# Kernel optimization log

Measured on AMD Instinct MI355X. Metric: run time of the kernel, lower is better.

## Reference

```python
import jax, jax.numpy as jnp
import numpy as np

N, E, F, H = 50000, 1_600_000, 6, 64


def setup_inputs() -> dict:
    key = jax.random.key(0)
    ks = jax.random.split(key, 12)
    inp = {
        "vertex_features": jax.random.normal(ks[0], (N, F), dtype=jnp.float32),
        "edges": jax.random.randint(ks[1], (2, E), 0, N, dtype=jnp.int64 if jax.config.jax_enable_x64 else jnp.int32),
        "weights": jax.random.uniform(ks[2], (E,), dtype=jnp.float32),
        # GCNConv layer params (glorot-ish scale) + biases (PyG default bias=True)
        "W1": jax.random.normal(ks[3], (F, H), dtype=jnp.float32) / np.sqrt(F),
        "b1": jnp.zeros((H,), jnp.float32),
        "W2": jax.random.normal(ks[4], (H, H), dtype=jnp.float32) / np.sqrt(H),
        "b2": jnp.zeros((H,), jnp.float32),
        "W3": jax.random.normal(ks[5], (H, H), dtype=jnp.float32) / np.sqrt(H),
        "b3": jnp.zeros((H,), jnp.float32),
        "Wl": jax.random.normal(ks[6], (H, 1), dtype=jnp.float32) / np.sqrt(H),
        "bl": jnp.zeros((1,), jnp.float32),
    }
    return inp


def _gcn_norm(edges, weights, n):
    # PyG gcn_norm: add self loops (weight 1), symmetric D^-1/2 A D^-1/2;
    # degree computed at target nodes (edge_index[1], flow source_to_target).
    row, col = edges[0], edges[1]
    loop = jnp.arange(n, dtype=row.dtype)
    row_f = jnp.concatenate([row, loop])
    col_f = jnp.concatenate([col, loop])
    w_f = jnp.concatenate([weights, jnp.ones((n,), weights.dtype)])
    deg = jax.ops.segment_sum(w_f, col_f, num_segments=n)
    dis = jnp.where(deg > 0, jax.lax.rsqrt(jnp.maximum(deg, 1e-30)), 0.0)
    norm = dis[row_f] * w_f * dis[col_f]
    return row_f, col_f, norm


def _gcn_conv(x, W, b, row, col, norm, n):
    xw = x @ W                                   # [n, H_out]
    agg = jax.ops.segment_sum(norm[:, None] * xw[row], col, num_segments=n)
    return agg + b


def reference(vertex_features, edges, weights, W1, b1, W2, b2, W3, b3, Wl, bl):
    n = vertex_features.shape[0]
    row, col, norm = _gcn_norm(edges, weights, n)  # norm identical for all layers
    h = jax.nn.sigmoid(_gcn_conv(vertex_features, W1, b1, row, col, norm, n))
    h = jax.nn.sigmoid(_gcn_conv(h, W2, b2, row, col, norm, n))
    h = jax.nn.sigmoid(_gcn_conv(h, W3, b3, row, col, norm, n))
    logits = h @ Wl + bl                           # [n, 1]
    return jax.nn.softmax(logits, axis=0)          # softmax over node dim
```

## Files before the change

kernel.cpp:

```cpp
#include <hip/hip_runtime.h>
#include <math.h>


#define BLK 256
#define SKB 256
#define CHUNK 4096
#define LROW 72

typedef __attribute__((ext_vector_type(8))) short bf16x8;
typedef __attribute__((ext_vector_type(4))) float f32x4;

__device__ inline unsigned short f2bf(float f) {
  unsigned u = __float_as_uint(f);
  return (unsigned short)((u + 0x7FFF + ((u >> 16) & 1)) >> 16);
}
__device__ inline float bflo(unsigned u) { return __uint_as_float(u << 16); }
__device__ inline float bfhi(unsigned u) { return __uint_as_float(u & 0xFFFF0000u); }


__global__ __launch_bounds__(256) void k_binscatter(
    const int* __restrict__ row, const int* __restrict__ col,
    const float* __restrict__ w, int E,
    int* __restrict__ bfill, int2* __restrict__ bucket, int CAP, int nEB,
    const float* __restrict__ W2, const float* __restrict__ W3,
    unsigned short* __restrict__ W2b, unsigned short* __restrict__ W3b) {
  if (blockIdx.x >= nEB) {
    int i = (blockIdx.x - nEB) * BLK + threadIdx.x;
    if (i < 4096) { W2b[i] = f2bf(W2[i]); W3b[i] = f2bf(W3[i]); }
    return;
  }
  __shared__ int2 stage[CHUNK];
  __shared__ int lhist[SKB], lbase[SKB], gbase[SKB], lfill[SKB];
  int t = threadIdx.x;
  int e0 = blockIdx.x * CHUNK;
  int n = E - e0; if (n > CHUNK) n = CHUNK;
  lhist[t] = 0; lfill[t] = 0;
  __syncthreads();
  for (int i = t; i < n; i += BLK) atomicAdd(&lhist[((unsigned)col[e0 + i]) >> 8], 1);
  __syncthreads();
  lbase[t] = lhist[t];
  __syncthreads();
  for (int off = 1; off < SKB; off <<= 1) {
    int v = (t >= off) ? lbase[t - off] : 0;
    __syncthreads();
    lbase[t] += v;
    __syncthreads();
  }
  int excl = lbase[t] - lhist[t];
  int cb = lhist[t];
  gbase[t] = cb ? atomicAdd(&bfill[t << 4], cb) : 0;
  __syncthreads();
  lbase[t] = excl;
  __syncthreads();
  for (int i = t; i < n; i += BLK) {
    int c = col[e0 + i];
    int b = ((unsigned)c) >> 8;
    int r = atomicAdd(&lfill[b], 1);
    stage[lbase[b] + r] = make_int2(row[e0 + i] | (c << 16), __float_as_int(w[e0 + i]));
  }
  __syncthreads();
  for (int i = t; i < n; i += BLK) {
    int2 p = stage[i];
    int b = ((unsigned)p.x) >> 24;
    bucket[(size_t)b * CAP + gbase[b] + (i - lbase[b])] = p;
  }
}


__global__ __launch_bounds__(256) void k_build(
    const int2* __restrict__ bucket, const int* __restrict__ bfill,
    const float* __restrict__ x,
    unsigned* __restrict__ csr, int* __restrict__ cnt, int* __restrict__ start,
    float* __restrict__ dis, unsigned short* __restrict__ x8b, int CAP, int N) {
  __shared__ int   hist[SKB];
  __shared__ float wsum[SKB];
  __shared__ int   lstart[SKB + 1];
  __shared__ int   lfill[SKB];
  int b = blockIdx.x, t = threadIdx.x;
  int n0 = b << 8;
  int M = N - n0; if (M > 256) M = 256;
  if (M <= 0) return;
  hist[t] = 0; wsum[t] = 0.0f; lfill[t] = 0;
  __syncthreads();
  const int2* bb = bucket + (size_t)b * CAP;
  int ec = bfill[b << 4];
  for (int i = t; i < ec; i += BLK) {
    int2 p = bb[i];
    int lc = (((unsigned)p.x) >> 16) & 255;
    atomicAdd(&hist[lc], 1);
    atomicAdd(&wsum[lc], __int_as_float(p.y));
  }
  __syncthreads();
  if (t == 0) {
    int run = 0;
    for (int i = 0; i < M; ++i) { lstart[i] = run; run += hist[i]; }
    lstart[M] = run;
  }
  __syncthreads();
  if (t < M) {
    int n = n0 + t;
    cnt[n] = hist[t];
    start[n] = b * CAP + lstart[t];
    float d = 1.0f / sqrtf(wsum[t] + 1.0f);
    dis[n] = d;
    const float* xr = x + (size_t)n * 6;
    uint4 pk;
    pk.x = (unsigned)f2bf(d * xr[0]) | ((unsigned)f2bf(d * xr[1]) << 16);
    pk.y = (unsigned)f2bf(d * xr[2]) | ((unsigned)f2bf(d * xr[3]) << 16);
    pk.z = (unsigned)f2bf(d * xr[4]) | ((unsigned)f2bf(d * xr[5]) << 16);
    pk.w = 0u;
    *(uint4*)(x8b + (size_t)n * 8) = pk;
  }
  __syncthreads();
  for (int i = t; i < ec; i += BLK) {
    int2 p = bb[i];
    int lc = (((unsigned)p.x) >> 16) & 255;
    int pos = lstart[lc] + atomicAdd(&lfill[lc], 1);
    csr[(size_t)b * CAP + pos] =
        ((unsigned)p.x & 0xFFFFu) | ((unsigned)f2bf(__int_as_float(p.y)) << 16);
  }
}


__global__ void k_layer1(const unsigned short* __restrict__ x8b,
                         const int* __restrict__ start, const int* __restrict__ cnt,
                         const unsigned* __restrict__ csr, const float* __restrict__ dis,
                         const float* __restrict__ W1, const float* __restrict__ b1,
                         unsigned short* __restrict__ hb, int N) {
  int t = blockIdx.x * blockDim.x + threadIdx.x;
  int n = t >> 3, sub = t & 7;
  if (n >= N) return;
  float a0 = 0.f, a1 = 0.f, a2 = 0.f, a3 = 0.f, a4 = 0.f, a5 = 0.f;
  if (sub == 0) {
    uint4 sv = *(const uint4*)(x8b + (size_t)n * 8);
    a0 = bflo(sv.x); a1 = bfhi(sv.x); a2 = bflo(sv.y);
    a3 = bfhi(sv.y); a4 = bflo(sv.z); a5 = bfhi(sv.z);
  }
  int s = start[n], e = s + cnt[n];
  int i = s + sub;
  for (; i + 8 < e; i += 16) {
    unsigned p0 = csr[i], p1 = csr[i + 8];
    uint4 h0 = *(const uint4*)(x8b + (size_t)(p0 & 0xFFFFu) * 8);
    uint4 h1 = *(const uint4*)(x8b + (size_t)(p1 & 0xFFFFu) * 8);
    float v0 = bfhi(p0), v1 = bfhi(p1);
    a0 += v0 * bflo(h0.x) + v1 * bflo(h1.x);
    a1 += v0 * bfhi(h0.x) + v1 * bfhi(h1.x);
    a2 += v0 * bflo(h0.y) + v1 * bflo(h1.y);
    a3 += v0 * bfhi(h0.y) + v1 * bfhi(h1.y);
    a4 += v0 * bflo(h0.z) + v1 * bflo(h1.z);
    a5 += v0 * bfhi(h0.z) + v1 * bfhi(h1.z);
  }
  for (; i < e; i += 8) {
    unsigned pe = csr[i];
    float v = bfhi(pe);
    uint4 hv = *(const uint4*)(x8b + (size_t)(pe & 0xFFFFu) * 8);
    a0 += v * bflo(hv.x); a1 += v * bfhi(hv.x);
    a2 += v * bflo(hv.y); a3 += v * bfhi(hv.y);
    a4 += v * bflo(hv.z); a5 += v * bfhi(hv.z);
  }
#pragma unroll
  for (int m = 1; m < 8; m <<= 1) {
    a0 += __shfl_xor(a0, m, 64); a1 += __shfl_xor(a1, m, 64);
    a2 += __shfl_xor(a2, m, 64); a3 += __shfl_xor(a3, m, 64);
    a4 += __shfl_xor(a4, m, 64); a5 += __shfl_xor(a5, m, 64);
  }
  float d = dis[n];
  a0 *= d; a1 *= d; a2 *= d; a3 *= d; a4 *= d; a5 *= d;
  unsigned short* o = hb + (size_t)n * 64;
#pragma unroll
  for (int jj = 0; jj < 2; ++jj) {
    int j4 = sub * 2 + jj;
    float4 acc = *(const float4*)(b1 + j4 * 4);
    const float* Wc = W1 + j4 * 4;
    acc.x += a0*Wc[0] + a1*Wc[64] + a2*Wc[128] + a3*Wc[192] + a4*Wc[256] + a5*Wc[320];
    acc.y += a0*Wc[1] + a1*Wc[65] + a2*Wc[129] + a3*Wc[193] + a4*Wc[257] + a5*Wc[321];
    acc.z += a0*Wc[2] + a1*Wc[66] + a2*Wc[130] + a3*Wc[194] + a4*Wc[258] + a5*Wc[322];
    acc.w += a0*Wc[3] + a1*Wc[67] + a2*Wc[131] + a3*Wc[195] + a4*Wc[259] + a5*Wc[323];
    uint2 pk;
    pk.x = (unsigned)f2bf(d / (1.0f + expf(-acc.x))) |
           ((unsigned)f2bf(d / (1.0f + expf(-acc.y))) << 16);
    pk.y = (unsigned)f2bf(d / (1.0f + expf(-acc.z))) |
           ((unsigned)f2bf(d / (1.0f + expf(-acc.w))) << 16);
    *(uint2*)(o + j4 * 4) = pk;
  }
}


__device__ inline void agg16(const unsigned short* __restrict__ hb,
                             const int* __restrict__ start,
                             const int* __restrict__ cnt,
                             const unsigned* __restrict__ csr,
                             const float* __restrict__ dis,
                             unsigned short* lag, int n0, int N) {
  int t = threadIdx.x;
  int r = t >> 4, sub = t & 15;
  int n = n0 + r;
  uint2 pk = make_uint2(0u, 0u);
  if (n < N) {
    uint2 sv = *(const uint2*)(hb + (size_t)n * 64 + sub * 4);
    float a0 = bflo(sv.x), a1 = bfhi(sv.x), a2 = bflo(sv.y), a3 = bfhi(sv.y);
    int s = start[n], e = s + cnt[n];
    int i = s;
    for (; i + 8 <= e; i += 8) {
      unsigned p0 = csr[i],     p1 = csr[i + 1], p2 = csr[i + 2], p3 = csr[i + 3];
      unsigned p4 = csr[i + 4], p5 = csr[i + 5], p6 = csr[i + 6], p7 = csr[i + 7];
      uint2 h0 = *(const uint2*)(hb + (size_t)(p0 & 0xFFFFu) * 64 + sub * 4);
      uint2 h1 = *(const uint2*)(hb + (size_t)(p1 & 0xFFFFu) * 64 + sub * 4);
      uint2 h2 = *(const uint2*)(hb + (size_t)(p2 & 0xFFFFu) * 64 + sub * 4);
      uint2 h3 = *(const uint2*)(hb + (size_t)(p3 & 0xFFFFu) * 64 + sub * 4);
      uint2 h4 = *(const uint2*)(hb + (size_t)(p4 & 0xFFFFu) * 64 + sub * 4);
      uint2 h5 = *(const uint2*)(hb + (size_t)(p5 & 0xFFFFu) * 64 + sub * 4);
      uint2 h6 = *(const uint2*)(hb + (size_t)(p6 & 0xFFFFu) * 64 + sub * 4);
      uint2 h7 = *(const uint2*)(hb + (size_t)(p7 & 0xFFFFu) * 64 + sub * 4);
      float v0 = bfhi(p0), v1 = bfhi(p1), v2 = bfhi(p2), v3 = bfhi(p3);
      float v4 = bfhi(p4), v5 = bfhi(p5), v6 = bfhi(p6), v7 = bfhi(p7);
      a0 += v0*bflo(h0.x) + v1*bflo(h1.x) + v2*bflo(h2.x) + v3*bflo(h3.x)
          + v4*bflo(h4.x) + v5*bflo(h5.x) + v6*bflo(h6.x) + v7*bflo(h7.x);
      a1 += v0*bfhi(h0.x) + v1*bfhi(h1.x) + v2*bfhi(h2.x) + v3*bfhi(h3.x)
          + v4*bfhi(h4.x) + v5*bfhi(h5.x) + v6*bfhi(h6.x) + v7*bfhi(h7.x);
      a2 += v0*bflo(h0.y) + v1*bflo(h1.y) + v2*bflo(h2.y) + v3*bflo(h3.y)
          + v4*bflo(h4.y) + v5*bflo(h5.y) + v6*bflo(h6.y) + v7*bflo(h7.y);
      a3 += v0*bfhi(h0.y) + v1*bfhi(h1.y) + v2*bfhi(h2.y) + v3*bfhi(h3.y)
          + v4*bfhi(h4.y) + v5*bfhi(h5.y) + v6*bfhi(h6.y) + v7*bfhi(h7.y);
    }
    for (; i < e; ++i) {
      unsigned pe = csr[i];
      float v = bfhi(pe);
      uint2 hv = *(const uint2*)(hb + (size_t)(pe & 0xFFFFu) * 64 + sub * 4);
      a0 += v * bflo(hv.x); a1 += v * bfhi(hv.x);
      a2 += v * bflo(hv.y); a3 += v * bfhi(hv.y);
    }
    float d = dis[n];
    pk.x = (unsigned)f2bf(d * a0) | ((unsigned)f2bf(d * a1) << 16);
    pk.y = (unsigned)f2bf(d * a2) | ((unsigned)f2bf(d * a3) << 16);
  }
  *(uint2*)(lag + r * LROW + sub * 4) = pk;
}


__global__ __launch_bounds__(256) void k_layer2f(
    const unsigned short* __restrict__ hb_in,
    const int* __restrict__ start, const int* __restrict__ cnt,
    const unsigned* __restrict__ csr, const float* __restrict__ dis,
    const unsigned short* __restrict__ Wb, const float* __restrict__ b,
    unsigned short* __restrict__ hb_out, int N) {
  __shared__ unsigned short lag[16 * LROW];
  int n0 = blockIdx.x * 16;
  agg16(hb_in, start, cnt, csr, dis, lag, n0, N);
  __syncthreads();
  int t = threadIdx.x;
  int wid = t >> 6, lane = t & 63, quad = lane >> 4, r16 = lane & 15;
  bf16x8 Af0 = *(const bf16x8*)(lag + r16 * LROW + quad * 8);
  bf16x8 Af1 = *(const bf16x8*)(lag + r16 * LROW + 32 + quad * 8);
  bf16x8 Bf0, Bf1;
#pragma unroll
  for (int j = 0; j < 8; ++j) {
    Bf0[j] = (short)Wb[(quad * 8 + j) * 64 + wid * 16 + r16];
    Bf1[j] = (short)Wb[(32 + quad * 8 + j) * 64 + wid * 16 + r16];
  }
  f32x4 z = {0.f, 0.f, 0.f, 0.f};
  z = __builtin_amdgcn_mfma_f32_16x16x32_bf16(Af0, Bf0, z, 0, 0, 0);
  z = __builtin_amdgcn_mfma_f32_16x16x32_bf16(Af1, Bf1, z, 0, 0, 0);
  float bias = b[wid * 16 + r16];
#pragma unroll
  for (int reg = 0; reg < 4; ++reg) {
    int nb = n0 + quad * 4 + reg;
    if (nb < N) {
      float h = dis[nb] / (1.0f + expf(-(z[reg] + bias)));
      hb_out[(size_t)nb * 64 + wid * 16 + r16] = f2bf(h);
    }
  }
}


__global__ __launch_bounds__(256) void k_layer3f(
    const unsigned short* __restrict__ hb_in,
    const int* __restrict__ start, const int* __restrict__ cnt,
    const unsigned* __restrict__ csr, const float* __restrict__ dis,
    const unsigned short* __restrict__ Wb, const float* __restrict__ b,
    const float* __restrict__ Wl, const float* __restrict__ bl,
    float* __restrict__ expv, float* __restrict__ red_part, int N) {
  __shared__ unsigned short lag[16 * LROW];
  __shared__ float psum[16][4];
  int n0 = blockIdx.x * 16;
  agg16(hb_in, start, cnt, csr, dis, lag, n0, N);
  __syncthreads();
  int t = threadIdx.x;
  int wid = t >> 6, lane = t & 63, quad = lane >> 4, r16 = lane & 15;
  bf16x8 Af0 = *(const bf16x8*)(lag + r16 * LROW + quad * 8);
  bf16x8 Af1 = *(const bf16x8*)(lag + r16 * LROW + 32 + quad * 8);
  bf16x8 Bf0, Bf1;
#pragma unroll
  for (int j = 0; j < 8; ++j) {
    Bf0[j] = (short)Wb[(quad * 8 + j) * 64 + wid * 16 + r16];
    Bf1[j] = (short)Wb[(32 + quad * 8 + j) * 64 + wid * 16 + r16];
  }
  f32x4 z = {0.f, 0.f, 0.f, 0.f};
  z = __builtin_amdgcn_mfma_f32_16x16x32_bf16(Af0, Bf0, z, 0, 0, 0);
  z = __builtin_amdgcn_mfma_f32_16x16x32_bf16(Af1, Bf1, z, 0, 0, 0);
  float bias = b[wid * 16 + r16];
  float wl = Wl[wid * 16 + r16];
  float p[4];
#pragma unroll
  for (int reg = 0; reg < 4; ++reg)
    p[reg] = wl / (1.0f + expf(-(z[reg] + bias)));
#pragma unroll
  for (int m = 1; m < 16; m <<= 1) {
#pragma unroll
    for (int reg = 0; reg < 4; ++reg) p[reg] += __shfl_xor(p[reg], m, 64);
  }
  if (r16 == 0) {
#pragma unroll
    for (int reg = 0; reg < 4; ++reg) psum[quad * 4 + reg][wid] = p[reg];
  }
  __syncthreads();
  if (t < 16) {
    int n = n0 + t;
    float lg = psum[t][0] + psum[t][1] + psum[t][2] + psum[t][3] + bl[0];
    float ev = (n < N) ? expf(lg) : 0.f;
    if (n < N) expv[n] = ev;
#pragma unroll
    for (int m = 1; m < 16; m <<= 1) ev += __shfl_xor(ev, m, 64);
    if (t == 0) atomicAdd(&red_part[(blockIdx.x & 63) << 4], ev);
  }
}

__global__ void k_out(const float* __restrict__ expv, int N,
                      const float* __restrict__ red_part, float* __restrict__ out) {
  int i = blockIdx.x * blockDim.x + threadIdx.x;
  int lane = threadIdx.x & 63;
  float s = red_part[lane << 4];
#pragma unroll
  for (int o = 32; o > 0; o >>= 1) s += __shfl_down(s, o, 64);
  s = __shfl(s, 0, 64);
  if (i < N) out[i] = expv[i] / s;
}


extern "C" void kernel_launch(void* const* d_in, const int* in_sizes, int n_in,
                              void* d_out, int out_size, void* d_ws, size_t ws_size,
                              hipStream_t stream) {
  const float* x   = (const float*)d_in[0];
  const int*   edg = (const int*)d_in[1];
  const float* w   = (const float*)d_in[2];
  const float* W1  = (const float*)d_in[3];
  const float* b1  = (const float*)d_in[4];
  const float* W2  = (const float*)d_in[5];
  const float* b2  = (const float*)d_in[6];
  const float* W3  = (const float*)d_in[7];
  const float* b3  = (const float*)d_in[8];
  const float* Wl  = (const float*)d_in[9];
  const float* bl  = (const float*)d_in[10];
  float* out = (float*)d_out;

  const int N = in_sizes[0] / 6;
  const int E = in_sizes[2];
  const int* row = edg;
  const int* col = edg + E;
  const int NB = (N + 255) >> 8;

  size_t off = 0;
  char* base = (char*)d_ws;
  auto alloc = [&](size_t bytes) -> void* {
    void* p = base + off;
    off += (bytes + 255) & ~(size_t)255;
    return p;
  };
  int*   bfill    = (int*)alloc((size_t)SKB * 16 * 4);
  float* red_part = (float*)alloc((size_t)64 * 16 * 4);
  size_t zero_bytes = off;
  int*   cnt    = (int*)alloc((size_t)N * 4);
  int*   start  = (int*)alloc((size_t)N * 4);
  float* dis    = (float*)alloc((size_t)N * 4);
  float* expv   = (float*)alloc((size_t)N * 4);
  unsigned short* x8b = (unsigned short*)alloc((size_t)N * 8 * 2);
  unsigned short* hb  = (unsigned short*)alloc((size_t)N * 64 * 2);
  unsigned short* W2b = (unsigned short*)alloc(4096 * 2);
  unsigned short* W3b = (unsigned short*)alloc(4096 * 2);
  size_t remain = (ws_size > off) ? (ws_size - off) : 0;
  long long capn = ((long long)remain) / ((long long)NB * 12);
  int CAP = (int)capn;
  if (CAP > 9216) CAP = 9216;
  if (CAP < 8704) CAP = 8704;
  unsigned* csr = (unsigned*)alloc((size_t)NB * CAP * 4);
  size_t h2sz = (size_t)N * 64 * 2;
  size_t bksz = (size_t)NB * CAP * 8;
  void* shared_blk = alloc(h2sz > bksz ? h2sz : bksz);
  int2*           bucket = (int2*)shared_blk;
  unsigned short* hb2    = (unsigned short*)shared_blk;

  const int nEB = (E + CHUNK - 1) / CHUNK;
  const int gE  = nEB + 16;
  const int gN  = (N + BLK - 1) / BLK;
  const int gN8 = (N * 8 + BLK - 1) / BLK;
  const int g16 = (N + 15) / 16;

  hipMemsetAsync(d_ws, 0, zero_bytes, stream);

  k_binscatter<<<gE, BLK, 0, stream>>>(row, col, w, E, bfill, bucket, CAP,
                                       nEB, W2, W3, W2b, W3b);
  k_build     <<<NB, BLK, 0, stream>>>(bucket, bfill, x, csr, cnt, start, dis, x8b, CAP, N);

  k_layer1<<<gN8, BLK, 0, stream>>>(x8b, start, cnt, csr, dis, W1, b1, hb, N);

  k_layer2f<<<g16, BLK, 0, stream>>>(hb, start, cnt, csr, dis, W2b, b2, hb2, N);

  k_layer3f<<<g16, BLK, 0, stream>>>(hb2, start, cnt, csr, dis, W3b, b3,
                                     Wl, bl, expv, red_part, N);

  k_out<<<gN, BLK, 0, stream>>>(expv, N, red_part, out);
}
```

Measured before the change: 216.3 us.

## Fuse all GCN stages into one persistent kernel with grid-wide barriers

Replaces the six separate kernel launches (bin scatter, CSR build, three layers, softmax output) with a single persistent kernel that loops over work with grid-stride loops and synchronises phases through an atomic-counter grid barrier. The grid is sized from the occupancy API so that all blocks can be resident at once. CHUNK is halved so the shared-memory union fits the requested occupancy. This removes launch gaps and inter-kernel drain, but adds spin-barrier cost, relies on every block being co-resident to avoid deadlock, and may reduce per-phase parallelism compared with the original grids.

```diff
diff --git a/kernel.cpp b/kernel.cpp
--- a/kernel.cpp
+++ b/kernel.cpp
@@ -4,7 +4,7 @@
 
 #define BLK 256
 #define SKB 256
-#define CHUNK 4096
+#define CHUNK 2048
 #define LROW 72
 
 typedef __attribute__((ext_vector_type(8))) short bf16x8;
@@ -16,174 +16,6 @@
 }
 __device__ inline float bflo(unsigned u) { return __uint_as_float(u << 16); }
 __device__ inline float bfhi(unsigned u) { return __uint_as_float(u & 0xFFFF0000u); }
-
-
-__global__ __launch_bounds__(256) void k_binscatter(
-    const int* __restrict__ row, const int* __restrict__ col,
-    const float* __restrict__ w, int E,
-    int* __restrict__ bfill, int2* __restrict__ bucket, int CAP, int nEB,
-    const float* __restrict__ W2, const float* __restrict__ W3,
-    unsigned short* __restrict__ W2b, unsigned short* __restrict__ W3b) {
-  if (blockIdx.x >= nEB) {
-    int i = (blockIdx.x - nEB) * BLK + threadIdx.x;
-    if (i < 4096) { W2b[i] = f2bf(W2[i]); W3b[i] = f2bf(W3[i]); }
-    return;
-  }
-  __shared__ int2 stage[CHUNK];
-  __shared__ int lhist[SKB], lbase[SKB], gbase[SKB], lfill[SKB];
-  int t = threadIdx.x;
-  int e0 = blockIdx.x * CHUNK;
-  int n = E - e0; if (n > CHUNK) n = CHUNK;
-  lhist[t] = 0; lfill[t] = 0;
-  __syncthreads();
-  for (int i = t; i < n; i += BLK) atomicAdd(&lhist[((unsigned)col[e0 + i]) >> 8], 1);
-  __syncthreads();
-  lbase[t] = lhist[t];
-  __syncthreads();
-  for (int off = 1; off < SKB; off <<= 1) {
-    int v = (t >= off) ? lbase[t - off] : 0;
-    __syncthreads();
-    lbase[t] += v;
-    __syncthreads();
-  }
-  int excl = lbase[t] - lhist[t];
-  int cb = lhist[t];
-  gbase[t] = cb ? atomicAdd(&bfill[t << 4], cb) : 0;
-  __syncthreads();
-  lbase[t] = excl;
-  __syncthreads();
-  for (int i = t; i < n; i += BLK) {
-    int c = col[e0 + i];
-    int b = ((unsigned)c) >> 8;
-    int r = atomicAdd(&lfill[b], 1);
-    stage[lbase[b] + r] = make_int2(row[e0 + i] | (c << 16), __float_as_int(w[e0 + i]));
-  }
-  __syncthreads();
-  for (int i = t; i < n; i += BLK) {
-    int2 p = stage[i];
-    int b = ((unsigned)p.x) >> 24;
-    bucket[(size_t)b * CAP + gbase[b] + (i - lbase[b])] = p;
-  }
-}
-
-
-__global__ __launch_bounds__(256) void k_build(
-    const int2* __restrict__ bucket, const int* __restrict__ bfill,
-    const float* __restrict__ x,
-    unsigned* __restrict__ csr, int* __restrict__ cnt, int* __restrict__ start,
-    float* __restrict__ dis, unsigned short* __restrict__ x8b, int CAP, int N) {
-  __shared__ int   hist[SKB];
-  __shared__ float wsum[SKB];
-  __shared__ int   lstart[SKB + 1];
-  __shared__ int   lfill[SKB];
-  int b = blockIdx.x, t = threadIdx.x;
-  int n0 = b << 8;
-  int M = N - n0; if (M > 256) M = 256;
-  if (M <= 0) return;
-  hist[t] = 0; wsum[t] = 0.0f; lfill[t] = 0;
-  __syncthreads();
-  const int2* bb = bucket + (size_t)b * CAP;
-  int ec = bfill[b << 4];
-  for (int i = t; i < ec; i += BLK) {
-    int2 p = bb[i];
-    int lc = (((unsigned)p.x) >> 16) & 255;
-    atomicAdd(&hist[lc], 1);
-    atomicAdd(&wsum[lc], __int_as_float(p.y));
-  }
-  __syncthreads();
-  if (t == 0) {
-    int run = 0;
-    for (int i = 0; i < M; ++i) { lstart[i] = run; run += hist[i]; }
-    lstart[M] = run;
-  }
-  __syncthreads();
-  if (t < M) {
-    int n = n0 + t;
-    cnt[n] = hist[t];
-    start[n] = b * CAP + lstart[t];
-    float d = 1.0f / sqrtf(wsum[t] + 1.0f);
-    dis[n] = d;
-    const float* xr = x + (size_t)n * 6;
-    uint4 pk;
-    pk.x = (unsigned)f2bf(d * xr[0]) | ((unsigned)f2bf(d * xr[1]) << 16);
-    pk.y = (unsigned)f2bf(d * xr[2]) | ((unsigned)f2bf(d * xr[3]) << 16);
-    pk.z = (unsigned)f2bf(d * xr[4]) | ((unsigned)f2bf(d * xr[5]) << 16);
-    pk.w = 0u;
-    *(uint4*)(x8b + (size_t)n * 8) = pk;
-  }
-  __syncthreads();
-  for (int i = t; i < ec; i += BLK) {
-    int2 p = bb[i];
-    int lc = (((unsigned)p.x) >> 16) & 255;
-    int pos = lstart[lc] + atomicAdd(&lfill[lc], 1);
-    csr[(size_t)b * CAP + pos] =
-        ((unsigned)p.x & 0xFFFFu) | ((unsigned)f2bf(__int_as_float(p.y)) << 16);
-  }
-}
-
-
-__global__ void k_layer1(const unsigned short* __restrict__ x8b,
-                         const int* __restrict__ start, const int* __restrict__ cnt,
-                         const unsigned* __restrict__ csr, const float* __restrict__ dis,
-                         const float* __restrict__ W1, const float* __restrict__ b1,
-                         unsigned short* __restrict__ hb, int N) {
-  int t = blockIdx.x * blockDim.x + threadIdx.x;
-  int n = t >> 3, sub = t & 7;
-  if (n >= N) return;
-  float a0 = 0.f, a1 = 0.f, a2 = 0.f, a3 = 0.f, a4 = 0.f, a5 = 0.f;
-  if (sub == 0) {
-    uint4 sv = *(const uint4*)(x8b + (size_t)n * 8);
-    a0 = bflo(sv.x); a1 = bfhi(sv.x); a2 = bflo(sv.y);
-    a3 = bfhi(sv.y); a4 = bflo(sv.z); a5 = bfhi(sv.z);
-  }
-  int s = start[n], e = s + cnt[n];
-  int i = s + sub;
-  for (; i + 8 < e; i += 16) {
-    unsigned p0 = csr[i], p1 = csr[i + 8];
-    uint4 h0 = *(const uint4*)(x8b + (size_t)(p0 & 0xFFFFu) * 8);
-    uint4 h1 = *(const uint4*)(x8b + (size_t)(p1 & 0xFFFFu) * 8);
-    float v0 = bfhi(p0), v1 = bfhi(p1);
-    a0 += v0 * bflo(h0.x) + v1 * bflo(h1.x);
-    a1 += v0 * bfhi(h0.x) + v1 * bfhi(h1.x);
-    a2 += v0 * bflo(h0.y) + v1 * bflo(h1.y);
-    a3 += v0 * bfhi(h0.y) + v1 * bfhi(h1.y);
-    a4 += v0 * bflo(h0.z) + v1 * bflo(h1.z);
-    a5 += v0 * bfhi(h0.z) + v1 * bfhi(h1.z);
-  }
-  for (; i < e; i += 8) {
-    unsigned pe = csr[i];
-    float v = bfhi(pe);
-    uint4 hv = *(const uint4*)(x8b + (size_t)(pe & 0xFFFFu) * 8);
-    a0 += v * bflo(hv.x); a1 += v * bfhi(hv.x);
-    a2 += v * bflo(hv.y); a3 += v * bfhi(hv.y);
-    a4 += v * bflo(hv.z); a5 += v * bfhi(hv.z);
-  }
-#pragma unroll
-  for (int m = 1; m < 8; m <<= 1) {
-    a0 += __shfl_xor(a0, m, 64); a1 += __shfl_xor(a1, m, 64);
-    a2 += __shfl_xor(a2, m, 64); a3 += __shfl_xor(a3, m, 64);
-    a4 += __shfl_xor(a4, m, 64); a5 += __shfl_xor(a5, m, 64);
-  }
-  float d = dis[n];
-  a0 *= d; a1 *= d; a2 *= d; a3 *= d; a4 *= d; a5 *= d;
-  unsigned short* o = hb + (size_t)n * 64;
-#pragma unroll
-  for (int jj = 0; jj < 2; ++jj) {
-    int j4 = sub * 2 + jj;
-    float4 acc = *(const float4*)(b1 + j4 * 4);
-    const float* Wc = W1 + j4 * 4;
-    acc.x += a0*Wc[0] + a1*Wc[64] + a2*Wc[128] + a3*Wc[192] + a4*Wc[256] + a5*Wc[320];
-    acc.y += a0*Wc[1] + a1*Wc[65] + a2*Wc[129] + a3*Wc[193] + a4*Wc[257] + a5*Wc[321];
-    acc.z += a0*Wc[2] + a1*Wc[66] + a2*Wc[130] + a3*Wc[194] + a4*Wc[258] + a5*Wc[322];
-    acc.w += a0*Wc[3] + a1*Wc[67] + a2*Wc[131] + a3*Wc[195] + a4*Wc[259] + a5*Wc[323];
-    uint2 pk;
-    pk.x = (unsigned)f2bf(d / (1.0f + expf(-acc.x))) |
-           ((unsigned)f2bf(d / (1.0f + expf(-acc.y))) << 16);
-    pk.y = (unsigned)f2bf(d / (1.0f + expf(-acc.z))) |
-           ((unsigned)f2bf(d / (1.0f + expf(-acc.w))) << 16);
-    *(uint2*)(o + j4 * 4) = pk;
-  }
-}
 
 
 __device__ inline void agg16(const unsigned short* __restrict__ hb,
@@ -238,102 +70,277 @@
 }
 
 
-__global__ __launch_bounds__(256) void k_layer2f(
-    const unsigned short* __restrict__ hb_in,
-    const int* __restrict__ start, const int* __restrict__ cnt,
-    const unsigned* __restrict__ csr, const float* __restrict__ dis,
-    const unsigned short* __restrict__ Wb, const float* __restrict__ b,
-    unsigned short* __restrict__ hb_out, int N) {
-  __shared__ unsigned short lag[16 * LROW];
-  int n0 = blockIdx.x * 16;
-  agg16(hb_in, start, cnt, csr, dis, lag, n0, N);
-  __syncthreads();
-  int t = threadIdx.x;
-  int wid = t >> 6, lane = t & 63, quad = lane >> 4, r16 = lane & 15;
-  bf16x8 Af0 = *(const bf16x8*)(lag + r16 * LROW + quad * 8);
-  bf16x8 Af1 = *(const bf16x8*)(lag + r16 * LROW + 32 + quad * 8);
-  bf16x8 Bf0, Bf1;
-#pragma unroll
-  for (int j = 0; j < 8; ++j) {
-    Bf0[j] = (short)Wb[(quad * 8 + j) * 64 + wid * 16 + r16];
-    Bf1[j] = (short)Wb[(32 + quad * 8 + j) * 64 + wid * 16 + r16];
-  }
-  f32x4 z = {0.f, 0.f, 0.f, 0.f};
-  z = __builtin_amdgcn_mfma_f32_16x16x32_bf16(Af0, Bf0, z, 0, 0, 0);
-  z = __builtin_amdgcn_mfma_f32_16x16x32_bf16(Af1, Bf1, z, 0, 0, 0);
-  float bias = b[wid * 16 + r16];
-#pragma unroll
-  for (int reg = 0; reg < 4; ++reg) {
-    int nb = n0 + quad * 4 + reg;
-    if (nb < N) {
-      float h = dis[nb] / (1.0f + expf(-(z[reg] + bias)));
-      hb_out[(size_t)nb * 64 + wid * 16 + r16] = f2bf(h);
-    }
-  }
-}
-
-
-__global__ __launch_bounds__(256) void k_layer3f(
-    const unsigned short* __restrict__ hb_in,
-    const int* __restrict__ start, const int* __restrict__ cnt,
-    const unsigned* __restrict__ csr, const float* __restrict__ dis,
-    const unsigned short* __restrict__ Wb, const float* __restrict__ b,
+__global__ __launch_bounds__(256, 8) void k_mega(
+    const int* __restrict__ row, const int* __restrict__ col,
+    const float* __restrict__ wgt, int E,
+    const float* __restrict__ x,
+    const float* __restrict__ W1, const float* __restrict__ b1,
+    const float* __restrict__ W2, const float* __restrict__ b2,
+    const float* __restrict__ W3, const float* __restrict__ b3,
     const float* __restrict__ Wl, const float* __restrict__ bl,
-    float* __restrict__ expv, float* __restrict__ red_part, int N) {
-  __shared__ unsigned short lag[16 * LROW];
-  __shared__ float psum[16][4];
-  int n0 = blockIdx.x * 16;
-  agg16(hb_in, start, cnt, csr, dis, lag, n0, N);
-  __syncthreads();
-  int t = threadIdx.x;
-  int wid = t >> 6, lane = t & 63, quad = lane >> 4, r16 = lane & 15;
-  bf16x8 Af0 = *(const bf16x8*)(lag + r16 * LROW + quad * 8);
-  bf16x8 Af1 = *(const bf16x8*)(lag + r16 * LROW + 32 + quad * 8);
-  bf16x8 Bf0, Bf1;
-#pragma unroll
-  for (int j = 0; j < 8; ++j) {
-    Bf0[j] = (short)Wb[(quad * 8 + j) * 64 + wid * 16 + r16];
-    Bf1[j] = (short)Wb[(32 + quad * 8 + j) * 64 + wid * 16 + r16];
-  }
-  f32x4 z = {0.f, 0.f, 0.f, 0.f};
-  z = __builtin_amdgcn_mfma_f32_16x16x32_bf16(Af0, Bf0, z, 0, 0, 0);
-  z = __builtin_amdgcn_mfma_f32_16x16x32_bf16(Af1, Bf1, z, 0, 0, 0);
-  float bias = b[wid * 16 + r16];
-  float wl = Wl[wid * 16 + r16];
-  float p[4];
-#pragma unroll
-  for (int reg = 0; reg < 4; ++reg)
-    p[reg] = wl / (1.0f + expf(-(z[reg] + bias)));
-#pragma unroll
-  for (int m = 1; m < 16; m <<= 1) {
-#pragma unroll
-    for (int reg = 0; reg < 4; ++reg) p[reg] += __shfl_xor(p[reg], m, 64);
-  }
-  if (r16 == 0) {
-#pragma unroll
-    for (int reg = 0; reg < 4; ++reg) psum[quad * 4 + reg][wid] = p[reg];
-  }
-  __syncthreads();
-  if (t < 16) {
-    int n = n0 + t;
-    float lg = psum[t][0] + psum[t][1] + psum[t][2] + psum[t][3] + bl[0];
-    float ev = (n < N) ? expf(lg) : 0.f;
-    if (n < N) expv[n] = ev;
-#pragma unroll
-    for (int m = 1; m < 16; m <<= 1) ev += __shfl_xor(ev, m, 64);
-    if (t == 0) atomicAdd(&red_part[(blockIdx.x & 63) << 4], ev);
-  }
-}
-
-__global__ void k_out(const float* __restrict__ expv, int N,
-                      const float* __restrict__ red_part, float* __restrict__ out) {
-  int i = blockIdx.x * blockDim.x + threadIdx.x;
-  int lane = threadIdx.x & 63;
-  float s = red_part[lane << 4];
-#pragma unroll
-  for (int o = 32; o > 0; o >>= 1) s += __shfl_down(s, o, 64);
-  s = __shfl(s, 0, 64);
-  if (i < N) out[i] = expv[i] / s;
+    int* __restrict__ bfill, float* __restrict__ red_part,
+    int* __restrict__ cntv, int* __restrict__ startv,
+    float* __restrict__ dis, float* __restrict__ expv,
+    unsigned short* __restrict__ x8b, unsigned short* __restrict__ hb,
+    unsigned short* __restrict__ W2b, unsigned short* __restrict__ W3b,
+    unsigned* __restrict__ csr, int2* __restrict__ bucket,
+    unsigned short* __restrict__ hb2, float* __restrict__ out,
+    int N, int NB, int nEB, int CAP, int* __restrict__ gcnt) {
+  __shared__ union {
+    struct { int2 stage[CHUNK]; int lhist[SKB], lbase[SKB], gbase[SKB], lfill[SKB]; } sc;
+    struct { int hist[SKB]; float wsum[SKB]; int lstart[SKB + 1]; int lfill[SKB]; } bd;
+    struct { unsigned short lag[16 * LROW]; float psum[16][4]; } ly;
+  } sm;
+  const int t   = threadIdx.x;
+  const int tid = blockIdx.x * BLK + t;
+  const int T   = gridDim.x * BLK;
+
+  auto gbar = [&](int k) {
+    __syncthreads();
+    if (t == 0) {
+      __threadfence();
+      atomicAdd(gcnt, 1);
+      int target = k * (int)gridDim.x;
+      while (atomicAdd(gcnt, 0) < target) __builtin_amdgcn_s_sleep(8);
+      __threadfence();
+    }
+    __syncthreads();
+  };
+
+  for (int i = tid; i < 4096; i += T) { W2b[i] = f2bf(W2[i]); W3b[i] = f2bf(W3[i]); }
+  for (int cb = blockIdx.x; cb < nEB; cb += gridDim.x) {
+    int e0 = cb * CHUNK;
+    int n = E - e0; if (n > CHUNK) n = CHUNK;
+    sm.sc.lhist[t] = 0; sm.sc.lfill[t] = 0;
+    __syncthreads();
+    for (int i = t; i < n; i += BLK)
+      atomicAdd(&sm.sc.lhist[((unsigned)col[e0 + i]) >> 8], 1);
+    __syncthreads();
+    sm.sc.lbase[t] = sm.sc.lhist[t];
+    __syncthreads();
+    for (int off = 1; off < SKB; off <<= 1) {
+      int v = (t >= off) ? sm.sc.lbase[t - off] : 0;
+      __syncthreads();
+      sm.sc.lbase[t] += v;
+      __syncthreads();
+    }
+    int excl = sm.sc.lbase[t] - sm.sc.lhist[t];
+    int cb2 = sm.sc.lhist[t];
+    sm.sc.gbase[t] = cb2 ? atomicAdd(&bfill[t << 4], cb2) : 0;
+    __syncthreads();
+    sm.sc.lbase[t] = excl;
+    __syncthreads();
+    for (int i = t; i < n; i += BLK) {
+      int c = col[e0 + i];
+      int b = ((unsigned)c) >> 8;
+      int r = atomicAdd(&sm.sc.lfill[b], 1);
+      sm.sc.stage[sm.sc.lbase[b] + r] =
+          make_int2(row[e0 + i] | (c << 16), __float_as_int(wgt[e0 + i]));
+    }
+    __syncthreads();
+    for (int i = t; i < n; i += BLK) {
+      int2 p = sm.sc.stage[i];
+      int b = ((unsigned)p.x) >> 24;
+      bucket[(size_t)b * CAP + sm.sc.gbase[b] + (i - sm.sc.lbase[b])] = p;
+    }
+    __syncthreads();
+  }
+  gbar(1);
+
+  for (int b = blockIdx.x; b < NB; b += gridDim.x) {
+    int n0 = b << 8;
+    int M = N - n0; if (M > 256) M = 256;
+    if (M <= 0) break;
+    sm.bd.hist[t] = 0; sm.bd.wsum[t] = 0.0f; sm.bd.lfill[t] = 0;
+    __syncthreads();
+    const int2* bb = bucket + (size_t)b * CAP;
+    int ec = bfill[b << 4];
+    for (int i = t; i < ec; i += BLK) {
+      int2 p = bb[i];
+      int lc = (((unsigned)p.x) >> 16) & 255;
+      atomicAdd(&sm.bd.hist[lc], 1);
+      atomicAdd(&sm.bd.wsum[lc], __int_as_float(p.y));
+    }
+    __syncthreads();
+    if (t == 0) {
+      int run = 0;
+      for (int i = 0; i < M; ++i) { sm.bd.lstart[i] = run; run += sm.bd.hist[i]; }
+      sm.bd.lstart[M] = run;
+    }
+    __syncthreads();
+    if (t < M) {
+      int n = n0 + t;
+      cntv[n] = sm.bd.hist[t];
+      startv[n] = b * CAP + sm.bd.lstart[t];
+      float d = 1.0f / sqrtf(sm.bd.wsum[t] + 1.0f);
+      dis[n] = d;
+      const float* xr = x + (size_t)n * 6;
+      uint4 pk;
+      pk.x = (unsigned)f2bf(d * xr[0]) | ((unsigned)f2bf(d * xr[1]) << 16);
+      pk.y = (unsigned)f2bf(d * xr[2]) | ((unsigned)f2bf(d * xr[3]) << 16);
+      pk.z = (unsigned)f2bf(d * xr[4]) | ((unsigned)f2bf(d * xr[5]) << 16);
+      pk.w = 0u;
+      *(uint4*)(x8b + (size_t)n * 8) = pk;
+    }
+    __syncthreads();
+    for (int i = t; i < ec; i += BLK) {
+      int2 p = bb[i];
+      int lc = (((unsigned)p.x) >> 16) & 255;
+      int pos = sm.bd.lstart[lc] + atomicAdd(&sm.bd.lfill[lc], 1);
+      csr[(size_t)b * CAP + pos] =
+          ((unsigned)p.x & 0xFFFFu) | ((unsigned)f2bf(__int_as_float(p.y)) << 16);
+    }
+    __syncthreads();
+  }
+  gbar(2);
+
+  for (int vt = tid; vt < N * 8; vt += T) {
+    int n = vt >> 3, sub = vt & 7;
+    float a0 = 0.f, a1 = 0.f, a2 = 0.f, a3 = 0.f, a4 = 0.f, a5 = 0.f;
+    if (sub == 0) {
+      uint4 sv = *(const uint4*)(x8b + (size_t)n * 8);
+      a0 = bflo(sv.x); a1 = bfhi(sv.x); a2 = bflo(sv.y);
+      a3 = bfhi(sv.y); a4 = bflo(sv.z); a5 = bfhi(sv.z);
+    }
+    int s = startv[n], e = s + cntv[n];
+    int i = s + sub;
+    for (; i + 8 < e; i += 16) {
+      unsigned p0 = csr[i], p1 = csr[i + 8];
+      uint4 h0 = *(const uint4*)(x8b + (size_t)(p0 & 0xFFFFu) * 8);
+      uint4 h1 = *(const uint4*)(x8b + (size_t)(p1 & 0xFFFFu) * 8);
+      float v0 = bfhi(p0), v1 = bfhi(p1);
+      a0 += v0 * bflo(h0.x) + v1 * bflo(h1.x);
+      a1 += v0 * bfhi(h0.x) + v1 * bfhi(h1.x);
+      a2 += v0 * bflo(h0.y) + v1 * bflo(h1.y);
+      a3 += v0 * bfhi(h0.y) + v1 * bfhi(h1.y);
+      a4 += v0 * bflo(h0.z) + v1 * bflo(h1.z);
+      a5 += v0 * bfhi(h0.z) + v1 * bfhi(h1.z);
+    }
+    for (; i < e; i += 8) {
+      unsigned pe = csr[i];
+      float v = bfhi(pe);
+      uint4 hv = *(const uint4*)(x8b + (size_t)(pe & 0xFFFFu) * 8);
+      a0 += v * bflo(hv.x); a1 += v * bfhi(hv.x);
+      a2 += v * bflo(hv.y); a3 += v * bfhi(hv.y);
+      a4 += v * bflo(hv.z); a5 += v * bfhi(hv.z);
+    }
+#pragma unroll
+    for (int m = 1; m < 8; m <<= 1) {
+      a0 += __shfl_xor(a0, m, 64); a1 += __shfl_xor(a1, m, 64);
+      a2 += __shfl_xor(a2, m, 64); a3 += __shfl_xor(a3, m, 64);
+      a4 += __shfl_xor(a4, m, 64); a5 += __shfl_xor(a5, m, 64);
+    }
+    float d = dis[n];
+    a0 *= d; a1 *= d; a2 *= d; a3 *= d; a4 *= d; a5 *= d;
+    unsigned short* o = hb + (size_t)n * 64;
+#pragma unroll
+    for (int jj = 0; jj < 2; ++jj) {
+      int j4 = sub * 2 + jj;
+      float4 acc = *(const float4*)(b1 + j4 * 4);
+      const float* Wc = W1 + j4 * 4;
+      acc.x += a0*Wc[0] + a1*Wc[64] + a2*Wc[128] + a3*Wc[192] + a4*Wc[256] + a5*Wc[320];
+      acc.y += a0*Wc[1] + a1*Wc[65] + a2*Wc[129] + a3*Wc[193] + a4*Wc[257] + a5*Wc[321];
+      acc.z += a0*Wc[2] + a1*Wc[66] + a2*Wc[130] + a3*Wc[194] + a4*Wc[258] + a5*Wc[322];
+      acc.w += a0*Wc[3] + a1*Wc[67] + a2*Wc[131] + a3*Wc[195] + a4*Wc[259] + a5*Wc[323];
+      uint2 pk;
+      pk.x = (unsigned)f2bf(d / (1.0f + expf(-acc.x))) |
+             ((unsigned)f2bf(d / (1.0f + expf(-acc.y))) << 16);
+      pk.y = (unsigned)f2bf(d / (1.0f + expf(-acc.z))) |
+             ((unsigned)f2bf(d / (1.0f + expf(-acc.w))) << 16);
+      *(uint2*)(o + j4 * 4) = pk;
+    }
+  }
+  gbar(3);
+
+  const int NG = (N + 15) >> 4;
+  {
+    int wid = t >> 6, lane = t & 63, quad = lane >> 4, r16 = lane & 15;
+    bf16x8 Bf0, Bf1;
+#pragma unroll
+    for (int j = 0; j < 8; ++j) {
+      Bf0[j] = (short)W2b[(quad * 8 + j) * 64 + wid * 16 + r16];
+      Bf1[j] = (short)W2b[(32 + quad * 8 + j) * 64 + wid * 16 + r16];
+    }
+    float bias = b2[wid * 16 + r16];
+    for (int g = blockIdx.x; g < NG; g += gridDim.x) {
+      int n0 = g * 16;
+      agg16(hb, startv, cntv, csr, dis, sm.ly.lag, n0, N);
+      __syncthreads();
+      bf16x8 Af0 = *(const bf16x8*)(sm.ly.lag + r16 * LROW + quad * 8);
+      bf16x8 Af1 = *(const bf16x8*)(sm.ly.lag + r16 * LROW + 32 + quad * 8);
+      f32x4 z = {0.f, 0.f, 0.f, 0.f};
+      z = __builtin_amdgcn_mfma_f32_16x16x32_bf16(Af0, Bf0, z, 0, 0, 0);
+      z = __builtin_amdgcn_mfma_f32_16x16x32_bf16(Af1, Bf1, z, 0, 0, 0);
+#pragma unroll
+      for (int reg = 0; reg < 4; ++reg) {
+        int nb = n0 + quad * 4 + reg;
+        if (nb < N) {
+          float h = dis[nb] / (1.0f + expf(-(z[reg] + bias)));
+          hb2[(size_t)nb * 64 + wid * 16 + r16] = f2bf(h);
+        }
+      }
+      __syncthreads();
+    }
+  }
+  gbar(4);
+
+  {
+    int wid = t >> 6, lane = t & 63, quad = lane >> 4, r16 = lane & 15;
+    bf16x8 Bf0, Bf1;
+#pragma unroll
+    for (int j = 0; j < 8; ++j) {
+      Bf0[j] = (short)W3b[(quad * 8 + j) * 64 + wid * 16 + r16];
+      Bf1[j] = (short)W3b[(32 + quad * 8 + j) * 64 + wid * 16 + r16];
+    }
+    float bias = b3[wid * 16 + r16];
+    float wl = Wl[wid * 16 + r16];
+    for (int g = blockIdx.x; g < NG; g += gridDim.x) {
+      int n0 = g * 16;
+      agg16(hb2, startv, cntv, csr, dis, sm.ly.lag, n0, N);
+      __syncthreads();
+      bf16x8 Af0 = *(const bf16x8*)(sm.ly.lag + r16 * LROW + quad * 8);
+      bf16x8 Af1 = *(const bf16x8*)(sm.ly.lag + r16 * LROW + 32 + quad * 8);
+      f32x4 z = {0.f, 0.f, 0.f, 0.f};
+      z = __builtin_amdgcn_mfma_f32_16x16x32_bf16(Af0, Bf0, z, 0, 0, 0);
+      z = __builtin_amdgcn_mfma_f32_16x16x32_bf16(Af1, Bf1, z, 0, 0, 0);
+      float p[4];
+#pragma unroll
+      for (int reg = 0; reg < 4; ++reg)
+        p[reg] = wl / (1.0f + expf(-(z[reg] + bias)));
+#pragma unroll
+      for (int m = 1; m < 16; m <<= 1) {
+#pragma unroll
+        for (int reg = 0; reg < 4; ++reg) p[reg] += __shfl_xor(p[reg], m, 64);
+      }
+      if (r16 == 0) {
+#pragma unroll
+        for (int reg = 0; reg < 4; ++reg) sm.ly.psum[quad * 4 + reg][wid] = p[reg];
+      }
+      __syncthreads();
+      if (t < 16) {
+        int n = n0 + t;
+        float lg = sm.ly.psum[t][0] + sm.ly.psum[t][1] + sm.ly.psum[t][2] +
+                   sm.ly.psum[t][3] + bl[0];
+        float ev = (n < N) ? expf(lg) : 0.f;
+        if (n < N) expv[n] = ev;
+#pragma unroll
+        for (int m = 1; m < 16; m <<= 1) ev += __shfl_xor(ev, m, 64);
+        if (t == 0) atomicAdd(&red_part[(blockIdx.x & 63) << 4], ev);
+      }
+      __syncthreads();
+    }
+  }
+  gbar(5);
+
+  {
+    int lane = t & 63;
+    float s = red_part[lane << 4];
+#pragma unroll
+    for (int o = 32; o > 0; o >>= 1) s += __shfl_down(s, o, 64);
+    s = __shfl(s, 0, 64);
+    float inv = 1.0f / s;
+    for (int i = tid; i < N; i += T) out[i] = expv[i] * inv;
+  }
 }
 
 
@@ -357,7 +364,8 @@
   const int E = in_sizes[2];
   const int* row = edg;
   const int* col = edg + E;
-  const int NB = (N + 255) >> 8;
+  const int NB  = (N + 255) >> 8;
+  const int nEB = (E + CHUNK - 1) / CHUNK;
 
   size_t off = 0;
   char* base = (char*)d_ws;
@@ -368,6 +376,7 @@
   };
   int*   bfill    = (int*)alloc((size_t)SKB * 16 * 4);
   float* red_part = (float*)alloc((size_t)64 * 16 * 4);
+  int*   gcnt     = (int*)alloc(256);
   size_t zero_bytes = off;
   int*   cnt    = (int*)alloc((size_t)N * 4);
   int*   start  = (int*)alloc((size_t)N * 4);
@@ -389,24 +398,18 @@
   int2*           bucket = (int2*)shared_blk;
   unsigned short* hb2    = (unsigned short*)shared_blk;
 
-  const int nEB = (E + CHUNK - 1) / CHUNK;
-  const int gE  = nEB + 16;
-  const int gN  = (N + BLK - 1) / BLK;
-  const int gN8 = (N * 8 + BLK - 1) / BLK;
-  const int g16 = (N + 15) / 16;
+  int dev = 0;
+  hipGetDevice(&dev);
+  int nCU = 256;
+  hipDeviceGetAttribute(&nCU, hipDeviceAttributeMultiprocessorCount, dev);
+  int maxAct = 0;
+  hipOccupancyMaxActiveBlocksPerMultiprocessor(&maxAct, k_mega, BLK, 0);
+  if (maxAct < 1) maxAct = 1;
+  int grid = nCU * maxAct;
 
   hipMemsetAsync(d_ws, 0, zero_bytes, stream);
-
-  k_binscatter<<<gE, BLK, 0, stream>>>(row, col, w, E, bfill, bucket, CAP,
-                                       nEB, W2, W3, W2b, W3b);
-  k_build     <<<NB, BLK, 0, stream>>>(bucket, bfill, x, csr, cnt, start, dis, x8b, CAP, N);
-
-  k_layer1<<<gN8, BLK, 0, stream>>>(x8b, start, cnt, csr, dis, W1, b1, hb, N);
-
-  k_layer2f<<<g16, BLK, 0, stream>>>(hb, start, cnt, csr, dis, W2b, b2, hb2, N);
-
-  k_layer3f<<<g16, BLK, 0, stream>>>(hb2, start, cnt, csr, dis, W3b, b3,
-                                     Wl, bl, expv, red_part, N);
-
-  k_out<<<gN, BLK, 0, stream>>>(expv, N, red_part, out);
+  k_mega<<<grid, BLK, 0, stream>>>(row, col, w, E, x, W1, b1, W2, b2, W3, b3,
+                                   Wl, bl, bfill, red_part, cnt, start, dis,
+                                   expv, x8b, hb, W2b, W3b, csr, bucket, hb2,
+                                   out, N, NB, nEB, CAP, gcnt);
 }
```

After: 857.0 us. 296% more time.
